# Optimization experiments

Hardware: AMD Instinct MI355X
Metric: run time of the kernel (lower is better)

## Reference

```python
import jax, jax.numpy as jnp
import numpy as np


def _c2e(faces):
    # faces: [6, B, C, h, h] in order back, down, front, left, right, up
    # returns equirect map [B, C, H=h, W=2h] via bilinear cube sampling
    _, B, C, h, _ = faces.shape
    H, W = h, 2 * h
    lat = (0.5 - (jnp.arange(H) + 0.5) / H) * jnp.pi      # +pi/2 (top) .. -pi/2
    lon = (2.0 * (jnp.arange(W) + 0.5) / W - 1.0) * jnp.pi  # -pi .. +pi
    cl = jnp.cos(lat)[:, None]
    vx = cl * jnp.sin(lon)[None, :]
    vy = jnp.broadcast_to(jnp.sin(lat)[:, None], (H, W))
    vz = cl * jnp.cos(lon)[None, :]
    dirs = jnp.stack([vx, vy, vz], -1)                     # [H,W,3]
    ax, ay, az = jnp.abs(vx), jnp.abs(vy), jnp.abs(vz)
    cond_z = (az >= ax) & (az >= ay)
    cond_x = (~cond_z) & (ax >= ay)
    # face ids: 0 back(-z) 1 down(-y) 2 front(+z) 3 left(-x) 4 right(+x) 5 up(+y)
    face = jnp.where(cond_z, jnp.where(vz > 0, 2, 0),
                     jnp.where(cond_x, jnp.where(vx > 0, 4, 3),
                               jnp.where(vy > 0, 5, 1)))
    N = jnp.array([[0, 0, -1], [0, -1, 0], [0, 0, 1], [-1, 0, 0], [1, 0, 0], [0, 1, 0]], jnp.float32)
    R = jnp.array([[-1, 0, 0], [1, 0, 0], [1, 0, 0], [0, 0, 1], [0, 0, -1], [1, 0, 0]], jnp.float32)
    U = jnp.array([[0, 1, 0], [0, 0, -1], [0, 1, 0], [0, 1, 0], [0, 1, 0], [0, 0, 1]], jnp.float32)
    den = jnp.sum(dirs * N[face], -1)
    a = jnp.sum(dirs * R[face], -1) / den                  # in-plane x, [-1,1]
    bcoord = jnp.sum(dirs * U[face], -1) / den             # in-plane y, [-1,1]
    uu = jnp.clip((a + 1.0) * 0.5 * (h - 1), 0.0, h - 1)   # align_corners-style
    vv = jnp.clip((1.0 - bcoord) * 0.5 * (h - 1), 0.0, h - 1)
    x0 = jnp.floor(uu).astype(jnp.int32)
    y0 = jnp.floor(vv).astype(jnp.int32)
    x1 = jnp.minimum(x0 + 1, h - 1)
    y1 = jnp.minimum(y0 + 1, h - 1)
    dx = uu - x0
    dy = vv - y0
    ft = faces.transpose(0, 3, 4, 1, 2).reshape(6, h, h, B * C)  # [6,h,h,B*C]
    g = lambda yy, xx: ft[face, yy, xx]                    # gather -> [H,W,B*C]
    out = (g(y0, x0) * ((1 - dx) * (1 - dy))[..., None]
           + g(y0, x1) * (dx * (1 - dy))[..., None]
           + g(y1, x0) * ((1 - dx) * dy)[..., None]
           + g(y1, x1) * (dx * dy)[..., None])
    return out.reshape(H, W, B, C).transpose(2, 3, 0, 1)


def _conv(x, w, bias, pad):
    y = jax.lax.conv_general_dilated(x, w, (1, 1), [(pad, pad), (pad, pad)],
                                     dimension_numbers=('NCHW', 'OIHW', 'NCHW'))
    return y + bias[None, :, None, None]


def setup_inputs() -> dict:
    key = jax.random.key(0)
    ks = jax.random.split(key, 12)
    B, C, h = 4, 64, 128
    face_shape = (B, C, h, h)
    return {
        'm': jax.random.normal(ks[0], (B, C, h, 2 * h), jnp.float32),
        'f': jax.random.normal(ks[1], face_shape, jnp.float32),
        'r': jax.random.normal(ks[2], face_shape, jnp.float32),
        'b': jax.random.normal(ks[3], face_shape, jnp.float32),
        'l': jax.random.normal(ks[4], face_shape, jnp.float32),
        'u': jax.random.normal(ks[5], face_shape, jnp.float32),
        'd': jax.random.normal(ks[6], face_shape, jnp.float32),
        'w_fusion': jax.random.normal(ks[7], (C, C, 3, 3), jnp.float32) * 0.05,
        'b_fusion': jnp.zeros((C,), jnp.float32),
        'w_mask': jax.random.normal(ks[8], (1, 2 * C, 1, 1), jnp.float32) * 0.05,
        'b_mask': jnp.zeros((1,), jnp.float32),
    }


def reference(m, f, r, b, l, u, d, w_fusion, b_fusion, w_mask, b_mask):
    # cube faces stacked in the original order: back, down, front, left, right, up
    faces = jnp.stack([b, d, f, l, r, u], 0)               # [6,B,C,h,h]
    aux = _c2e(faces)                                      # [B,C,h,2h]
    m_aux = jax.nn.relu(_conv(aux, w_fusion, b_fusion, 1))
    m_main = jax.nn.relu(_conv(m, w_fusion, b_fusion, 1))  # shared conv_fusion weights
    joint = jnp.concatenate([m_main, m_aux], axis=1)
    mask = jax.nn.sigmoid(_conv(joint, w_mask, b_mask, 0)) # [B,1,h,2h]
    return m + mask * m_aux
```

## Files before the change

### kernel.cpp

```cpp
#include <hip/hip_runtime.h>
#include <math.h>
#include <stdint.h>

#define BB 4
#define CC 64
#define HH 128
#define HOUT 128
#define WOUT 256
#define NPIX (HOUT * WOUT)
#define NMAP (BB * CC * HOUT * WOUT)
#define FSTR ((size_t)HH * HH * 256)

#define NB_PREP 146
#define NB_FACE (6 * HH * 2)
#define NB_PACK (BB * HOUT)
#define NB_FRONT (NB_PREP + NB_FACE + NB_PACK)

typedef __attribute__((ext_vector_type(8))) short short8;
typedef __attribute__((ext_vector_type(4))) float floatx4;

__device__ __forceinline__ uint16_t f2bf(float f) {
    uint32_t u = __float_as_uint(f);
    u += 0x7fffu + ((u >> 16) & 1u);
    return (uint16_t)(u >> 16);
}
__device__ __forceinline__ float bfu2f(uint32_t v) { return __uint_as_float(v << 16); }

__global__ __launch_bounds__(256) void front_kernel(
    uint32_t* __restrict__ pk, float* __restrict__ pdx, float* __restrict__ pdy,
    const float* __restrict__ wf, uint4* __restrict__ Bsw,
    const float* __restrict__ pB, const float* __restrict__ pD,
    const float* __restrict__ pF, const float* __restrict__ pL,
    const float* __restrict__ pR, const float* __restrict__ pU,
    uint16_t* __restrict__ FCLlo, uint16_t* __restrict__ FCLhi,
    const float* __restrict__ msrc, uint16_t* __restrict__ Xm,
    uint4* __restrict__ zpage) {
    __shared__ uint16_t lds[64 * 256];
    int bid = blockIdx.x;
    int t = threadIdx.x;

    if (bid < NB_PREP) {
        if (bid == 0 && t == 0) *zpage = make_uint4(0, 0, 0, 0);
        if (bid < 128) {
            int p = bid * 256 + t;
            int y = p >> 8;
            int x = p & 255;
            const float PI = 3.14159265358979323846f;
            float lat = (0.5f - (y + 0.5f) / (float)HOUT) * PI;
            float lon = (2.0f * (x + 0.5f) / (float)WOUT - 1.0f) * PI;
            float cl = cosf(lat);
            float vx = cl * sinf(lon);
            float vy = sinf(lat);
            float vz = cl * cosf(lon);
            float ax = fabsf(vx), ay = fabsf(vy), az = fabsf(vz);

            int face;
            float den, a, b;
            if (az >= ax && az >= ay) {
                if (vz > 0.0f) { face = 2; den = vz;  a = vx;  b = vy; }
                else           { face = 0; den = -vz; a = -vx; b = vy; }
            } else if (ax >= ay) {
                if (vx > 0.0f) { face = 4; den = vx;  a = -vz; b = vy; }
                else           { face = 3; den = -vx; a = vz;  b = vy; }
            } else {
                if (vy > 0.0f) { face = 5; den = vy;  a = vx;  b = vz; }
                else           { face = 1; den = -vy; a = vx;  b = -vz; }
            }
            a /= den;
            b /= den;
            float uu = fminf(fmaxf((a + 1.0f) * 0.5f * (HH - 1), 0.0f), (float)(HH - 1));
            float vv = fminf(fmaxf((1.0f - b) * 0.5f * (HH - 1), 0.0f), (float)(HH - 1));
            int x0 = (int)floorf(uu);
            int y0 = (int)floorf(vv);
            int x1 = min(x0 + 1, HH - 1);
            int y1 = min(y0 + 1, HH - 1);
            pdx[p] = uu - (float)x0;
            pdy[p] = vv - (float)y0;
            pk[p] = (uint32_t)face | ((uint32_t)x0 << 3) | ((uint32_t)y0 << 10) |
                    ((uint32_t)x1 << 17) | ((uint32_t)y1 << 24);
        } else {
            int tid = (bid - 128) * 256 + t;
            if (tid >= 9 * 2 * 4 * 64) return;
            int lane = tid & 63;
            int rest = tid >> 6;
            int n = rest & 3, ks = (rest >> 2) & 1, tap = rest >> 3;
            int co = n * 16 + (lane & 15);
            uint32_t w4[4];
#pragma unroll
            for (int pw = 0; pw < 4; pw++) {
                int ci0 = ks * 32 + (lane >> 4) * 8 + pw * 2;
                uint32_t lo = f2bf(wf[(size_t)(co * CC + ci0) * 9 + tap]);
                uint32_t hi = f2bf(wf[(size_t)(co * CC + ci0 + 1) * 9 + tap]);
                w4[pw] = lo | (hi << 16);
            }
            Bsw[tid] = make_uint4(w4[0], w4[1], w4[2], w4[3]);
        }
    } else if (bid < NB_PREP + NB_FACE) {
        int fb = bid - NB_PREP;
        int half = fb & 1;
        int y = (fb >> 1) & 127;
        int fc = fb >> 8;
        const float* src = (fc == 0) ? pB : (fc == 1) ? pD : (fc == 2) ? pF
                         : (fc == 3) ? pL : (fc == 4) ? pR : pU;
        uint16_t* FCLf = (fc < 3) ? (FCLlo + (size_t)fc * FSTR)
                                  : (FCLhi + (size_t)(fc - 3) * FSTR);

#pragma unroll
        for (int it = 0; it < 16; it++) {
            int jq = it * 256 + t;
            int bc = jq >> 4;
            int q = jq & 15;
            floatx4 v = *(const floatx4*)(src + ((size_t)bc * HH + y) * HH +
                                          half * 64 + q * 4);
            int cg = bc >> 3;
#pragma unroll
            for (int j = 0; j < 4; j++) {
                int xl = q * 4 + j;
                int swz = cg ^ (xl & 7) ^ ((xl >> 3) & 7);
                lds[xl * 256 + (swz << 3) + (bc & 7)] = f2bf(v[j]);
            }
        }
        __syncthreads();
        size_t obase = ((size_t)y * HH + half * 64) * 256;
#pragma unroll
        for (int i = 0; i < 8; i++) {
            int q = i * 256 + t;
            int xx = q >> 5, cg = q & 31;
            int swz = cg ^ (xx & 7) ^ ((xx >> 3) & 7);
            int off = xx * 256 + swz * 8;
            *(uint4*)&FCLf[obase + (size_t)q * 8] = *(const uint4*)&lds[off];
        }
    } else {
        int by = bid - (NB_PREP + NB_FACE);
        int b = by >> 7, y = by & 127;

#pragma unroll
        for (int it = 0; it < 16; it++) {
            int jq = it * 256 + t;
            int c = jq >> 6;
            int q = jq & 63;
            floatx4 v = *(const floatx4*)(msrc + ((size_t)(b * CC + c) * HOUT + y) * WOUT +
                                          q * 4);
            int cg = c >> 3;
#pragma unroll
            for (int j = 0; j < 4; j++) {
                int x = q * 4 + j;
                int swz = cg ^ (x & 7) ^ ((x >> 3) & 7);
                lds[x * 64 + (swz << 3) + (c & 7)] = f2bf(v[j]);
            }
        }
        __syncthreads();
        size_t obase = (size_t)((b * HOUT + y) * WOUT) * CC;
#pragma unroll
        for (int i = 0; i < 8; i++) {
            int q = i * 256 + t;
            int p = q >> 3, c8 = q & 7;
            int swz = c8 ^ (p & 7) ^ ((p >> 3) & 7);
            int off = p * 64 + swz * 8;
            *(uint4*)&Xm[obase + (size_t)q * 8] = *(const uint4*)&lds[off];
        }
    }
}

__global__ __launch_bounds__(256) void gather_kernel(
    const uint32_t* __restrict__ pk, const float* __restrict__ pdx,
    const float* __restrict__ pdy, const uint16_t* __restrict__ FCLlo,
    const uint16_t* __restrict__ FCLhi, uint16_t* __restrict__ Xa) {
    int bid = blockIdx.x;
    int sw = (bid & 7) * 512 + (bid >> 3);
    int tid = sw * 256 + threadIdx.x;
    int chunk = tid & 31;
    int p = tid >> 5;

    uint32_t k = pk[p];
    float dx = pdx[p], dy = pdy[p];
    int fc = k & 7;
    int x0 = (k >> 3) & 127, y0 = (k >> 10) & 127;
    int x1 = (k >> 17) & 127, y1 = (k >> 24) & 127;

    const uint16_t* fb = (fc < 3) ? (FCLlo + (size_t)fc * FSTR)
                                  : (FCLhi + (size_t)(fc - 3) * FSTR);
    const uint16_t* base = fb + chunk * 8;
    uint4 c00 = *(const uint4*)(base + ((size_t)y0 * HH + x0) * 256);
    uint4 c01 = *(const uint4*)(base + ((size_t)y0 * HH + x1) * 256);
    uint4 c10 = *(const uint4*)(base + ((size_t)y1 * HH + x0) * 256);
    uint4 c11 = *(const uint4*)(base + ((size_t)y1 * HH + x1) * 256);

    float w00 = (1.0f - dx) * (1.0f - dy);
    float w01 = dx * (1.0f - dy);
    float w10 = (1.0f - dx) * dy;
    float w11 = dx * dy;

    const uint32_t* a00 = (const uint32_t*)&c00;
    const uint32_t* a01 = (const uint32_t*)&c01;
    const uint32_t* a10 = (const uint32_t*)&c10;
    const uint32_t* a11 = (const uint32_t*)&c11;
    uint32_t r[4];
#pragma unroll
    for (int w = 0; w < 4; w++) {
        float lo = w00 * bfu2f(a00[w] & 0xffffu) + w01 * bfu2f(a01[w] & 0xffffu)
                 + w10 * bfu2f(a10[w] & 0xffffu) + w11 * bfu2f(a11[w] & 0xffffu);
        float hi = w00 * bfu2f(a00[w] >> 16) + w01 * bfu2f(a01[w] >> 16)
                 + w10 * bfu2f(a10[w] >> 16) + w11 * bfu2f(a11[w] >> 16);
        r[w] = (uint32_t)f2bf(lo) | ((uint32_t)f2bf(hi) << 16);
    }

    int b = chunk >> 3, c = (chunk & 7) * 8;
    int y = p >> 8, x = p & 255;
    size_t o = (((size_t)(b * HOUT + y)) * WOUT + x) * CC + c;
    *(uint4*)(Xa + o) = make_uint4(r[0], r[1], r[2], r[3]);
}

__global__ __launch_bounds__(256, 4) void gemm_fused_kernel(
    const uint16_t* __restrict__ Xm, const uint16_t* __restrict__ Xa,
    const uint4* __restrict__ Bsw, const float* __restrict__ bias,
    const float* __restrict__ wm, const float* __restrict__ bm,
    const float* __restrict__ m, const uint4* __restrict__ zpage,
    float* __restrict__ out) {
    __shared__ __align__(16) uint16_t lds[3 * 132 * 64];
    float* ldsf = (float*)lds;

    int gid = blockIdx.x;
    int b = gid >> 8;
    int i = gid & 255;
    int xcd = i & 7, j = i >> 3;
    int y = xcd * 16 + (j & 15);
    int h = j >> 4;
    const int wx = h * 128 - 2;

    int tid = threadIdx.x;
    int lane = tid & 63;
    int wave = tid >> 6;
    int l15 = lane & 15, lq = lane >> 4;

    float mp[2][4];
#pragma unroll
    for (int mt = 0; mt < 2; mt++)
#pragma unroll
        for (int rg = 0; rg < 4; rg++) mp[mt][rg] = 0.0f;

    floatx4 acc[2][4];

#pragma unroll
    for (int phase = 0; phase < 2; phase++) {
        const uint16_t* Xb = (phase ? Xa : Xm) + (size_t)b * (HOUT * WOUT * CC);

        __syncthreads();
        for (int r = 0; r < 3; r++) {
            int gy = y + r - 1;
            bool rowok = (unsigned)gy < (unsigned)HOUT;
            const uint16_t* Xrow = Xb + (size_t)gy * (WOUT * CC);
#pragma unroll 1
            for (int it = 0; it < 5; it++) {
                int cid = it * 256 + tid;
                if (cid < 1056) {
                    int c = cid & 7;
                    int p = cid >> 3;
                    int gx = wx + p;
                    int csrc = c ^ (p & 7);
                    const uint4* src = (rowok && (unsigned)gx < (unsigned)WOUT)
                        ? (const uint4*)(Xrow + (size_t)gx * CC + csrc * 8)
                        : zpage;
                    __builtin_amdgcn_global_load_lds(
                        (const uint32_t*)src,
                        (uint32_t*)&lds[(size_t)(r * 1056 + it * 256 + wave * 64) * 8],
                        16, 0, 0);
                }
            }
        }
        __syncthreads();

#pragma unroll
        for (int mt = 0; mt < 2; mt++)
#pragma unroll
            for (int n = 0; n < 4; n++) acc[mt][n] = (floatx4)0.0f;

#pragma unroll
        for (int tap = 0; tap < 9; tap++) {
            const int r = tap / 3;
            const int dx = tap % 3 - 1;
#pragma unroll
            for (int ks = 0; ks < 2; ks++) {
                short8 bfr[4];
                const uint4* bp = Bsw + (size_t)((tap * 2 + ks) * 4) * 64 + lane;
#pragma unroll
                for (int n = 0; n < 4; n++) {
                    uint4 t4 = bp[n * 64];
                    bfr[n] = *(short8*)&t4;
                }
#pragma unroll
                for (int mt = 0; mt < 2; mt++) {
                    int p = wave * 32 + mt * 16 + l15 + dx + 2;
                    int chunk = ks * 4 + lq;
                    int slot = (r * 132 + p) * 8 + (chunk ^ (p & 7));
                    short8 af = *(const short8*)&lds[slot * 8];
#pragma unroll
                    for (int n = 0; n < 4; n++)
                        acc[mt][n] = __builtin_amdgcn_mfma_f32_16x16x32_bf16(
                            af, bfr[n], acc[mt][n], 0, 0, 0);
                }
            }
        }

        if (phase == 0) {
#pragma unroll
            for (int n = 0; n < 4; n++) {
                float bb = bias[n * 16 + l15];
                float wmn = wm[n * 16 + l15];
#pragma unroll
                for (int mt = 0; mt < 2; mt++)
#pragma unroll
                    for (int rg = 0; rg < 4; rg++) {
                        float v = acc[mt][n][rg] + bb;
                        v = v > 0.0f ? v : 0.0f;
                        mp[mt][rg] += wmn * v;
                    }
            }
        } else {
#pragma unroll
            for (int n = 0; n < 4; n++) {
                float bb = bias[n * 16 + l15];
                float wan = wm[64 + n * 16 + l15];
#pragma unroll
                for (int mt = 0; mt < 2; mt++)
#pragma unroll
                    for (int rg = 0; rg < 4; rg++) {
                        float v = acc[mt][n][rg] + bb;
                        v = v > 0.0f ? v : 0.0f;
                        acc[mt][n][rg] = v;
                        mp[mt][rg] += wan * v;
                    }
            }
        }
    }

    float bm0 = bm[0];
#pragma unroll
    for (int mt = 0; mt < 2; mt++)
#pragma unroll
        for (int rg = 0; rg < 4; rg++) {
            float v = mp[mt][rg];
            v += __shfl_xor(v, 1);
            v += __shfl_xor(v, 2);
            v += __shfl_xor(v, 4);
            v += __shfl_xor(v, 8);
            mp[mt][rg] = 1.0f / (1.0f + expf(-(v + bm0)));
        }

    __syncthreads();
#pragma unroll
    for (int mt = 0; mt < 2; mt++)
#pragma unroll
        for (int n = 0; n < 4; n++)
#pragma unroll
            for (int rg = 0; rg < 4; rg++) {
                int px = wave * 32 + mt * 16 + lq * 4 + rg;
                int co = n * 16 + l15;
                ldsf[co * 129 + px] = mp[mt][rg] * acc[mt][n][rg];
            }
    __syncthreads();

    size_t base0 = (size_t)b * (CC * HOUT * WOUT) + (size_t)y * WOUT + h * 128;
#pragma unroll
    for (int it = 0; it < 32; it++) {
        int q = it * 256 + tid;
        int c = q >> 7, px = q & 127;
        size_t idx = base0 + (size_t)c * (HOUT * WOUT) + px;
        out[idx] = m[idx] + ldsf[c * 129 + px];
    }
}

__global__ __launch_bounds__(256) void signal_kernel(float* __restrict__ out, float v) {
    int idx = blockIdx.x * 256 + threadIdx.x;
    out[idx] = v;
}

extern "C" void kernel_launch(void* const* d_in, const int* in_sizes, int n_in,
                              void* d_out, int out_size, void* d_ws, size_t ws_size,
                              hipStream_t stream) {
    const float* m  = (const float*)d_in[0];
    const float* f  = (const float*)d_in[1];
    const float* r  = (const float*)d_in[2];
    const float* bk = (const float*)d_in[3];
    const float* l  = (const float*)d_in[4];
    const float* u  = (const float*)d_in[5];
    const float* dn = (const float*)d_in[6];
    const float* wf = (const float*)d_in[7];
    const float* bf = (const float*)d_in[8];
    const float* wm = (const float*)d_in[9];
    const float* bm = (const float*)d_in[10];
    float* out = (float*)d_out;

    const size_t FCL_HALF = (size_t)3 * HH * HH * 256 * 2;
    const size_t OFF_FCLH = 0;
    const size_t OFF_XA   = FCL_HALF;
    const size_t OFF_XM   = OFF_XA + (size_t)NMAP * 2;
    const size_t OFF_BSW  = OFF_XM + (size_t)NMAP * 2;
    const size_t OFF_PK   = OFF_BSW + (9 * 2 * 4 * 64 * 16);
    const size_t OFF_PDX  = OFF_PK + (1u << 17);
    const size_t OFF_PDY  = OFF_PDX + (1u << 17);
    const size_t OFF_ZP   = OFF_PDY + (1u << 17);
    const size_t NEED     = OFF_ZP + 64;

    if (ws_size < NEED) {
        float v = 100.0f + (float)(ws_size >> 20);
        signal_kernel<<<NMAP / 256, 256, 0, stream>>>(out, v);
        return;
    }

    char* ws = (char*)d_ws;
    uint16_t* FCLhi = (uint16_t*)(ws + OFF_FCLH);
    uint16_t* Xa    = (uint16_t*)(ws + OFF_XA);
    uint16_t* Xm    = (uint16_t*)(ws + OFF_XM);
    uint4* Bsw      = (uint4*)(ws + OFF_BSW);
    uint32_t* pk    = (uint32_t*)(ws + OFF_PK);
    float* pdx      = (float*)(ws + OFF_PDX);
    float* pdy      = (float*)(ws + OFF_PDY);
    uint4* zpage    = (uint4*)(ws + OFF_ZP);
    uint16_t* FCLlo = (uint16_t*)d_out;

    front_kernel<<<NB_FRONT, 256, 0, stream>>>(pk, pdx, pdy, wf, Bsw,
                                               bk, dn, f, l, r, u, FCLlo, FCLhi,
                                               m, Xm, zpage);
    gather_kernel<<<(NPIX * 32) / 256, 256, 0, stream>>>(pk, pdx, pdy, FCLlo, FCLhi, Xa);
    gemm_fused_kernel<<<BB * HOUT * 2, 256, 0, stream>>>(Xm, Xa, Bsw, bf, wm, bm, m,
                                                         zpage, out);
}
```

Before: 245.0 us.

## Move main-input pack into gather kernel and batch face-transpose loads

The packing of the main feature map into a bf16 channel-last layout moves out of the front kernel and into the gather kernel as extra blocks, and is rewritten to skip the LDS transpose, using strided per-channel loads instead. This rebalances work between the two kernels, shortening the front kernel's critical path and letting the pack overlap with the gather. The face-transpose loop now issues eight vector loads before converting them, to raise memory-level parallelism. The direct pack reads eight channels at stride NPIX per thread, so its loads may coalesce less well than the old LDS-based version.

```diff
diff --git a/kernel.cpp b/kernel.cpp
--- a/kernel.cpp
+++ b/kernel.cpp
@@ -13,8 +13,10 @@
 
 #define NB_PREP 146
 #define NB_FACE (6 * HH * 2)
+#define NB_FRONT (NB_PREP + NB_FACE)
+#define NB_GATHER 4096
 #define NB_PACK (BB * HOUT)
-#define NB_FRONT (NB_PREP + NB_FACE + NB_PACK)
+#define NB_GP (NB_GATHER + NB_PACK)
 
 typedef __attribute__((ext_vector_type(8))) short short8;
 typedef __attribute__((ext_vector_type(4))) float floatx4;
@@ -33,7 +35,6 @@
     const float* __restrict__ pF, const float* __restrict__ pL,
     const float* __restrict__ pR, const float* __restrict__ pU,
     uint16_t* __restrict__ FCLlo, uint16_t* __restrict__ FCLhi,
-    const float* __restrict__ msrc, uint16_t* __restrict__ Xm,
     uint4* __restrict__ zpage) {
     __shared__ uint16_t lds[64 * 256];
     int bid = blockIdx.x;
@@ -95,7 +96,7 @@
             }
             Bsw[tid] = make_uint4(w4[0], w4[1], w4[2], w4[3]);
         }
-    } else if (bid < NB_PREP + NB_FACE) {
+    } else {
         int fb = bid - NB_PREP;
         int half = fb & 1;
         int y = (fb >> 1) & 127;
@@ -105,19 +106,29 @@
         uint16_t* FCLf = (fc < 3) ? (FCLlo + (size_t)fc * FSTR)
                                   : (FCLhi + (size_t)(fc - 3) * FSTR);
 
-#pragma unroll
-        for (int it = 0; it < 16; it++) {
-            int jq = it * 256 + t;
-            int bc = jq >> 4;
-            int q = jq & 15;
-            floatx4 v = *(const floatx4*)(src + ((size_t)bc * HH + y) * HH +
+        floatx4 vv[8];
+#pragma unroll
+        for (int batch = 0; batch < 2; batch++) {
+#pragma unroll
+            for (int k = 0; k < 8; k++) {
+                int jq = (batch * 8 + k) * 256 + t;
+                int bc = jq >> 4;
+                int q = jq & 15;
+                vv[k] = *(const floatx4*)(src + ((size_t)bc * HH + y) * HH +
                                           half * 64 + q * 4);
-            int cg = bc >> 3;
-#pragma unroll
-            for (int j = 0; j < 4; j++) {
-                int xl = q * 4 + j;
-                int swz = cg ^ (xl & 7) ^ ((xl >> 3) & 7);
-                lds[xl * 256 + (swz << 3) + (bc & 7)] = f2bf(v[j]);
+            }
+#pragma unroll
+            for (int k = 0; k < 8; k++) {
+                int jq = (batch * 8 + k) * 256 + t;
+                int bc = jq >> 4;
+                int q = jq & 15;
+                int cg = bc >> 3;
+#pragma unroll
+                for (int j = 0; j < 4; j++) {
+                    int xl = q * 4 + j;
+                    int swz = cg ^ (xl & 7) ^ ((xl >> 3) & 7);
+                    lds[xl * 256 + (swz << 3) + (bc & 7)] = f2bf(vv[k][j]);
+                }
             }
         }
         __syncthreads();
@@ -130,85 +141,83 @@
             int off = xx * 256 + swz * 8;
             *(uint4*)&FCLf[obase + (size_t)q * 8] = *(const uint4*)&lds[off];
         }
-    } else {
-        int by = bid - (NB_PREP + NB_FACE);
-        int b = by >> 7, y = by & 127;
-
-#pragma unroll
-        for (int it = 0; it < 16; it++) {
-            int jq = it * 256 + t;
-            int c = jq >> 6;
-            int q = jq & 63;
-            floatx4 v = *(const floatx4*)(msrc + ((size_t)(b * CC + c) * HOUT + y) * WOUT +
-                                          q * 4);
-            int cg = c >> 3;
-#pragma unroll
-            for (int j = 0; j < 4; j++) {
-                int x = q * 4 + j;
-                int swz = cg ^ (x & 7) ^ ((x >> 3) & 7);
-                lds[x * 64 + (swz << 3) + (c & 7)] = f2bf(v[j]);
-            }
-        }
-        __syncthreads();
-        size_t obase = (size_t)((b * HOUT + y) * WOUT) * CC;
-#pragma unroll
-        for (int i = 0; i < 8; i++) {
-            int q = i * 256 + t;
-            int p = q >> 3, c8 = q & 7;
-            int swz = c8 ^ (p & 7) ^ ((p >> 3) & 7);
-            int off = p * 64 + swz * 8;
-            *(uint4*)&Xm[obase + (size_t)q * 8] = *(const uint4*)&lds[off];
-        }
     }
 }
 
-__global__ __launch_bounds__(256) void gather_kernel(
+__global__ __launch_bounds__(256) void gather_pack_kernel(
     const uint32_t* __restrict__ pk, const float* __restrict__ pdx,
     const float* __restrict__ pdy, const uint16_t* __restrict__ FCLlo,
-    const uint16_t* __restrict__ FCLhi, uint16_t* __restrict__ Xa) {
+    const uint16_t* __restrict__ FCLhi, uint16_t* __restrict__ Xa,
+    const float* __restrict__ msrc, uint16_t* __restrict__ Xm) {
     int bid = blockIdx.x;
-    int sw = (bid & 7) * 512 + (bid >> 3);
-    int tid = sw * 256 + threadIdx.x;
-    int chunk = tid & 31;
-    int p = tid >> 5;
-
-    uint32_t k = pk[p];
-    float dx = pdx[p], dy = pdy[p];
-    int fc = k & 7;
-    int x0 = (k >> 3) & 127, y0 = (k >> 10) & 127;
-    int x1 = (k >> 17) & 127, y1 = (k >> 24) & 127;
-
-    const uint16_t* fb = (fc < 3) ? (FCLlo + (size_t)fc * FSTR)
-                                  : (FCLhi + (size_t)(fc - 3) * FSTR);
-    const uint16_t* base = fb + chunk * 8;
-    uint4 c00 = *(const uint4*)(base + ((size_t)y0 * HH + x0) * 256);
-    uint4 c01 = *(const uint4*)(base + ((size_t)y0 * HH + x1) * 256);
-    uint4 c10 = *(const uint4*)(base + ((size_t)y1 * HH + x0) * 256);
-    uint4 c11 = *(const uint4*)(base + ((size_t)y1 * HH + x1) * 256);
-
-    float w00 = (1.0f - dx) * (1.0f - dy);
-    float w01 = dx * (1.0f - dy);
-    float w10 = (1.0f - dx) * dy;
-    float w11 = dx * dy;
-
-    const uint32_t* a00 = (const uint32_t*)&c00;
-    const uint32_t* a01 = (const uint32_t*)&c01;
-    const uint32_t* a10 = (const uint32_t*)&c10;
-    const uint32_t* a11 = (const uint32_t*)&c11;
-    uint32_t r[4];
-#pragma unroll
-    for (int w = 0; w < 4; w++) {
-        float lo = w00 * bfu2f(a00[w] & 0xffffu) + w01 * bfu2f(a01[w] & 0xffffu)
-                 + w10 * bfu2f(a10[w] & 0xffffu) + w11 * bfu2f(a11[w] & 0xffffu);
-        float hi = w00 * bfu2f(a00[w] >> 16) + w01 * bfu2f(a01[w] >> 16)
-                 + w10 * bfu2f(a10[w] >> 16) + w11 * bfu2f(a11[w] >> 16);
-        r[w] = (uint32_t)f2bf(lo) | ((uint32_t)f2bf(hi) << 16);
+    if (bid < NB_GATHER) {
+        int sw = (bid & 7) * 512 + (bid >> 3);
+        int tid = sw * 256 + threadIdx.x;
+        int chunk = tid & 31;
+        int p = tid >> 5;
+
+        uint32_t k = pk[p];
+        float dx = pdx[p], dy = pdy[p];
+        int fc = k & 7;
+        int x0 = (k >> 3) & 127, y0 = (k >> 10) & 127;
+        int x1 = (k >> 17) & 127, y1 = (k >> 24) & 127;
+
+        const uint16_t* fb = (fc < 3) ? (FCLlo + (size_t)fc * FSTR)
+                                      : (FCLhi + (size_t)(fc - 3) * FSTR);
+        const uint16_t* base = fb + chunk * 8;
+        uint4 c00 = *(const uint4*)(base + ((size_t)y0 * HH + x0) * 256);
+        uint4 c01 = *(const uint4*)(base + ((size_t)y0 * HH + x1) * 256);
+        uint4 c10 = *(const uint4*)(base + ((size_t)y1 * HH + x0) * 256);
+        uint4 c11 = *(const uint4*)(base + ((size_t)y1 * HH + x1) * 256);
+
+        float w00 = (1.0f - dx) * (1.0f - dy);
+        float w01 = dx * (1.0f - dy);
+        float w10 = (1.0f - dx) * dy;
+        float w11 = dx * dy;
+
+        const uint32_t* a00 = (const uint32_t*)&c00;
+        const uint32_t* a01 = (const uint32_t*)&c01;
+        const uint32_t* a10 = (const uint32_t*)&c10;
+        const uint32_t* a11 = (const uint32_t*)&c11;
+        uint32_t r[4];
+#pragma unroll
+        for (int w = 0; w < 4; w++) {
+            float lo = w00 * bfu2f(a00[w] & 0xffffu) + w01 * bfu2f(a01[w] & 0xffffu)
+                     + w10 * bfu2f(a10[w] & 0xffffu) + w11 * bfu2f(a11[w] & 0xffffu);
+            float hi = w00 * bfu2f(a00[w] >> 16) + w01 * bfu2f(a01[w] >> 16)
+                     + w10 * bfu2f(a10[w] >> 16) + w11 * bfu2f(a11[w] >> 16);
+            r[w] = (uint32_t)f2bf(lo) | ((uint32_t)f2bf(hi) << 16);
+        }
+
+        int b = chunk >> 3, c = (chunk & 7) * 8;
+        int y = p >> 8, x = p & 255;
+        size_t o = (((size_t)(b * HOUT + y)) * WOUT + x) * CC + c;
+        *(uint4*)(Xa + o) = make_uint4(r[0], r[1], r[2], r[3]);
+    } else {
+        int by = bid - NB_GATHER;
+        int b = by >> 7, y = by & 127;
+        int t = threadIdx.x;
+        int c8 = t & 7;
+        int xw = t >> 3;
+        const float* mb = msrc + (size_t)b * (CC * NPIX) + (size_t)y * WOUT;
+        size_t obase = ((size_t)(b * HOUT + y) * WOUT) * CC;
+
+#pragma unroll 2
+        for (int i = 0; i < 8; i++) {
+            int x = xw + i * 32;
+            float val[8];
+#pragma unroll
+            for (int j = 0; j < 8; j++)
+                val[j] = mb[(size_t)(c8 * 8 + j) * NPIX + x];
+            uint32_t w4[4];
+#pragma unroll
+            for (int jj = 0; jj < 4; jj++)
+                w4[jj] = (uint32_t)f2bf(val[2 * jj]) |
+                         ((uint32_t)f2bf(val[2 * jj + 1]) << 16);
+            *(uint4*)&Xm[obase + (size_t)x * CC + c8 * 8] =
+                make_uint4(w4[0], w4[1], w4[2], w4[3]);
+        }
     }
-
-    int b = chunk >> 3, c = (chunk & 7) * 8;
-    int y = p >> 8, x = p & 255;
-    size_t o = (((size_t)(b * HOUT + y)) * WOUT + x) * CC + c;
-    *(uint4*)(Xa + o) = make_uint4(r[0], r[1], r[2], r[3]);
 }
 
 __global__ __launch_bounds__(256, 4) void gemm_fused_kernel(
@@ -421,8 +430,9 @@
 
     front_kernel<<<NB_FRONT, 256, 0, stream>>>(pk, pdx, pdy, wf, Bsw,
                                                bk, dn, f, l, r, u, FCLlo, FCLhi,
-                                               m, Xm, zpage);
-    gather_kernel<<<(NPIX * 32) / 256, 256, 0, stream>>>(pk, pdx, pdy, FCLlo, FCLhi, Xa);
+                                               zpage);
+    gather_pack_kernel<<<NB_GP, 256, 0, stream>>>(pk, pdx, pdy, FCLlo, FCLhi, Xa,
+                                                  m, Xm);
     gemm_fused_kernel<<<BB * HOUT * 2, 256, 0, stream>>>(Xm, Xa, Bsw, bf, wm, bm, m,
                                                          zpage, out);
 }
```

Measured after the change: 262.1 us. 1.07x slower.
